# Optimization experiments

Hardware: AMD Instinct MI355X
Metric: run time of the kernel (lower is better)

The kernel has to match this reference:

```python
import jax, jax.numpy as jnp
import numpy as np

N = 50000      # total nodes across batch of graphs
E = 800000     # total directed edges (avg degree 16)
B = 64         # number of graphs
D = 128        # input_dim == hidden_dim
L = 4          # num_layers - 1 GIN layers
OUT = 10
BN_EPS = 1e-5


def setup_inputs() -> dict:
    key = jax.random.key(0)
    ks = jax.random.split(key, 12)
    s = 0.05
    return {
        "x": jax.random.normal(ks[0], (N, D), jnp.float32),
        "pi": jax.random.uniform(ks[1], (B, 25), jnp.float32),
        "eps": jnp.zeros((L,), jnp.float32),
        "mlp_w1": jax.random.normal(ks[2], (L, D, D), jnp.float32) * s,
        "mlp_b1": jnp.zeros((L, D), jnp.float32),
        "mlp_bn_g": jnp.ones((L, D), jnp.float32),
        "mlp_bn_b": jnp.zeros((L, D), jnp.float32),
        "mlp_w2": jax.random.normal(ks[3], (L, D, D), jnp.float32) * s,
        "mlp_b2": jnp.zeros((L, D), jnp.float32),
        "bn_g": jnp.ones((L, D), jnp.float32),
        "bn_b": jnp.zeros((L, D), jnp.float32),
        "attend_w": jax.random.normal(ks[4], (D * (L + 1), 1), jnp.float32) * s,
        "attend_b": jnp.zeros((1,), jnp.float32),
        "pi_w": jax.random.normal(ks[5], (25, 16), jnp.float32) * s,
        "pi_b": jnp.zeros((16,), jnp.float32),
        "out_w": jax.random.normal(ks[6], (D * (L + 1) + 16, OUT), jnp.float32) * s,
        "out_b": jnp.zeros((OUT,), jnp.float32),
        "edge_index": jax.random.randint(ks[7], (2, E), 0, N, dtype=jnp.int32),
        "graph_id": jnp.sort(jax.random.randint(ks[8], (N,), 0, B, dtype=jnp.int32)),
    }


def _bn(z, g, b):
    # BatchNorm1d in training mode over all nodes (axis 0)
    m = z.mean(axis=0)
    v = z.var(axis=0)
    return (z - m) * jax.lax.rsqrt(v + BN_EPS) * g + b


def reference(x, pi, eps, mlp_w1, mlp_b1, mlp_bn_g, mlp_bn_b, mlp_w2, mlp_b2,
              bn_g, bn_b, attend_w, attend_b, pi_w, pi_b, out_w, out_b,
              edge_index, graph_id):
    src, dst = edge_index[0], edge_index[1]
    h = x
    reps = [x]
    for l in range(L):
        # GIN sum aggregation (learn_eps=True: no self-loops in Adj)
        pooled = jax.ops.segment_sum(h[src], dst, num_segments=N)
        pooled = pooled + (1.0 + eps[l]) * h
        # 2-layer MLP: Linear -> BN -> ReLU -> Linear
        z = jax.nn.relu(_bn(pooled @ mlp_w1[l] + mlp_b1[l], mlp_bn_g[l], mlp_bn_b[l]))
        z = z @ mlp_w2[l] + mlp_b2[l]
        # outer BN + ReLU
        h = jax.nn.relu(_bn(z, bn_g[l], bn_b[l]))
        reps.append(h)
    hr = jnp.concatenate(reps, axis=1)               # [N, D*(L+1)]
    # per-graph attention softmax over nodes
    scores = (hr @ attend_w + attend_b)[:, 0]        # [N]
    smax = jax.ops.segment_max(scores, graph_id, num_segments=B)
    e = jnp.exp(scores - smax[graph_id])
    denom = jax.ops.segment_sum(e, graph_id, num_segments=B)
    coef = e / denom[graph_id]
    gemb = jax.ops.segment_sum(hr * coef[:, None], graph_id, num_segments=B)  # [B, D*(L+1)]
    # persistence-image branch (PI computed host-side; treated as input)
    pie = jax.nn.relu(pi @ pi_w + pi_b)              # [B, 16]
    feat = jnp.concatenate([gemb, pie], axis=1)      # [B, D*(L+1)+16]
    return feat @ out_w + out_b                      # [B, OUT]
```

## Files before the change

### kernel.cpp

```cpp
#include <hip/hip_runtime.h>
#include <hip/hip_bf16.h>

#define NN 50000
#define EE 800000
#define BBG 64
#define DD 128
#define LLAY 4
#define HRW 640
#define NOUT 10
#define NXCD 8
#define NBUCK 196
#define BUCKCAP 4608
#define EB 250
#define ECH 3200

typedef __hip_bfloat16 bf16;
typedef __attribute__((ext_vector_type(8))) short short8;
typedef __attribute__((ext_vector_type(4))) float f32x4;

__device__ __forceinline__ float b2f(bf16 v) { return __bfloat162float(v); }
__device__ __forceinline__ float bflo(unsigned u) { return __uint_as_float(u << 16); }
__device__ __forceinline__ float bfhi(unsigned u) { return __uint_as_float(u & 0xffff0000u); }
__device__ __forceinline__ unsigned short f2bs(float v) {
  bf16 h = __float2bfloat16(v);
  unsigned short r; __builtin_memcpy(&r, &h, 2); return r;
}
__device__ __forceinline__ int dtype_of(const void* __restrict__ bng) {
  return (*(const unsigned*)bng == 0x3F800000u) ? 1 : 0;
}
__device__ __forceinline__ float ldf(const void* __restrict__ p, long i, int dt) {
  return dt ? ((const float*)p)[i] : b2f(((const bf16*)p)[i]);
}

__device__ __forceinline__ int xccid() {
  unsigned v;
  asm("s_getreg_b32 %0, hwreg(HW_REG_XCC_ID)" : "=s"(v));
  return (int)(v & (NXCD - 1));
}

__device__ __forceinline__ void fadd_l2(float* p, float v) {
  asm volatile("global_atomic_add_f32 %0, %1, off" :: "v"(p), "v"(v) : "memory");
}

__device__ __forceinline__ int lower_bound_i(const int* __restrict__ a, int n, int key) {
  int lo = 0, hi = n;
  while (lo < hi) { int mid = (lo + hi) >> 1; if (a[mid] < key) lo = mid + 1; else hi = mid; }
  return lo;
}

__global__ __launch_bounds__(256) void gnn_init(const void* __restrict__ x,
                                                bf16* __restrict__ hrb,
                                                const void* __restrict__ w1,
                                                const void* __restrict__ w2,
                                                bf16* __restrict__ w1t,
                                                bf16* __restrict__ w2t,
                                                const void* __restrict__ aw,
                                                float* __restrict__ scores,
                                                const int* __restrict__ ei,
                                                int* __restrict__ bucketCnt,
                                                unsigned* __restrict__ bucketStore,
                                                const void* __restrict__ bng) {
  int dt = dtype_of(bng);
  int tid = threadIdx.x;
  if (blockIdx.x >= 3375) {
    int i = (blockIdx.x - 3375) * 256 + tid;
    int l = i >> 14, rem = i & 16383, n = rem >> 7, k = rem & 127;
    long src = (long)l * 16384 + k * 128 + n;
    w1t[i] = __float2bfloat16(ldf(w1, src, dt));
    w2t[i] = __float2bfloat16(ldf(w2, src, dt));
    return;
  }
  if (blockIdx.x >= 3125) {
    __shared__ int lcnt[NBUCK], gbase[NBUCK];
    int bb = blockIdx.x - 3125;
    int base = bb * ECH;
    if (tid < NBUCK) lcnt[tid] = 0;
    __syncthreads();
    #pragma unroll
    for (int j = 0; j < 13; j++) {
      int k = j * 256 + tid;
      if (k < ECH) {
        int dst = ei[EE + base + k];
        atomicAdd(&lcnt[dst >> 8], 1);
      }
    }
    __syncthreads();
    if (tid < NBUCK) {
      gbase[tid] = atomicAdd(&bucketCnt[tid * 16], lcnt[tid]);
      lcnt[tid] = 0;
    }
    __syncthreads();
    #pragma unroll
    for (int j = 0; j < 13; j++) {
      int k = j * 256 + tid;
      if (k < ECH) {
        int e = base + k;
        int src = ei[e];
        int dst = ei[EE + e];
        int b = dst >> 8;
        int r = atomicAdd(&lcnt[b], 1);
        bucketStore[b * BUCKCAP + gbase[b] + r] =
            (unsigned)src | ((unsigned)(dst & 255) << 16);
      }
    }
    return;
  }
  int n = blockIdx.x * 16 + (tid >> 4);
  int il = tid & 15;
  long base = (long)n * DD + il * 8;
  float v[8];
  if (dt) {
    float4 a0 = *(const float4*)((const float*)x + base);
    float4 a1 = *(const float4*)((const float*)x + base + 4);
    v[0] = a0.x; v[1] = a0.y; v[2] = a0.z; v[3] = a0.w;
    v[4] = a1.x; v[5] = a1.y; v[6] = a1.z; v[7] = a1.w;
  } else {
    uint4 u = *(const uint4*)((const bf16*)x + base);
    v[0] = bflo(u.x); v[1] = bfhi(u.x); v[2] = bflo(u.y); v[3] = bfhi(u.y);
    v[4] = bflo(u.z); v[5] = bfhi(u.z); v[6] = bflo(u.w); v[7] = bfhi(u.w);
  }
  uint4 o;
  o.x = (unsigned)f2bs(v[0]) | ((unsigned)f2bs(v[1]) << 16);
  o.y = (unsigned)f2bs(v[2]) | ((unsigned)f2bs(v[3]) << 16);
  o.z = (unsigned)f2bs(v[4]) | ((unsigned)f2bs(v[5]) << 16);
  o.w = (unsigned)f2bs(v[6]) | ((unsigned)f2bs(v[7]) << 16);
  *(uint4*)(hrb + (size_t)n * HRW + il * 8) = o;
  float ss = 0.f;
  #pragma unroll
  for (int k = 0; k < 8; k++) ss += v[k] * ldf(aw, il * 8 + k, dt);
  ss += __shfl_xor(ss, 1, 64); ss += __shfl_xor(ss, 2, 64);
  ss += __shfl_xor(ss, 4, 64); ss += __shfl_xor(ss, 8, 64);
  if (il == 0) scores[n] = ss;
}

__global__ __launch_bounds__(256) void gnn_csr(const int* __restrict__ bucketCnt,
                                               const unsigned* __restrict__ bucketStore,
                                               int* __restrict__ rowstart,
                                               int* __restrict__ csr_src) {
  __shared__ int cnt[256], dbase[256], buf[256];
  int b = blockIdx.x, tid = threadIdx.x;
  int p = (tid < b) ? bucketCnt[tid * 16] : 0;
  buf[tid] = p;
  __syncthreads();
  for (int s = 128; s > 0; s >>= 1) {
    if (tid < s) buf[tid] += buf[tid + s];
    __syncthreads();
  }
  int start = buf[0];
  int sz = bucketCnt[b * 16];
  __syncthreads();
  cnt[tid] = 0;
  __syncthreads();
  for (int j = 0; j < 18; j++) {
    int k = j * 256 + tid;
    if (k < sz) atomicAdd(&cnt[bucketStore[b * BUCKCAP + k] >> 16], 1);
  }
  __syncthreads();
  int c = cnt[tid];
  buf[tid] = c;
  __syncthreads();
  for (int ofs = 1; ofs < 256; ofs <<= 1) {
    int t = (tid >= ofs) ? buf[tid - ofs] : 0;
    __syncthreads();
    buf[tid] += t;
    __syncthreads();
  }
  dbase[tid] = buf[tid] - c;
  int d = b * 256 + tid;
  if (d <= NN) rowstart[d] = start + buf[tid] - c;
  cnt[tid] = 0;
  __syncthreads();
  for (int j = 0; j < 18; j++) {
    int k = j * 256 + tid;
    if (k < sz) {
      unsigned v = bucketStore[b * BUCKCAP + k];
      int dlo = v >> 16;
      int r = atomicAdd(&cnt[dlo], 1);
      csr_src[start + dbase[dlo] + r] = (int)(v & 0xFFFFu);
    }
  }
}

__device__ __forceinline__ void acc8(float* a, uint4 u) {
  a[0] += bflo(u.x); a[1] += bfhi(u.x);
  a[2] += bflo(u.y); a[3] += bfhi(u.y);
  a[4] += bflo(u.z); a[5] += bfhi(u.z);
  a[6] += bflo(u.w); a[7] += bfhi(u.w);
}

__device__ __forceinline__ float2 statsum(const float* __restrict__ stat, int c) {
  float s = 0.f, q = 0.f;
  #pragma unroll
  for (int k = 0; k < 8; k++) { s += stat[k * 256 + c]; q += stat[k * 256 + 128 + c]; }
  return make_float2(s, q);
}

__global__ __launch_bounds__(512) void gnn_gmg1(const bf16* __restrict__ hrb, int l,
                                                const int* __restrict__ rowstart,
                                                const int* __restrict__ csr_src,
                                                const void* __restrict__ eps,
                                                const bf16* __restrict__ Wt,
                                                const void* __restrict__ bias, int biasOfs,
                                                bf16* __restrict__ out,
                                                float* __restrict__ statOut,
                                                const void* __restrict__ bng) {
  int dt = dtype_of(bng);
  __shared__ __align__(16) unsigned ar[16][68];
  __shared__ int qhead;
  int tid = threadIdx.x, lane = tid & 63;
  int w = tid >> 6;
  int q = lane >> 4, il = lane & 15;
  int r0 = blockIdx.x * 16;
  const bf16* stripe = hrb + l * DD;
  float s = 1.0f + ldf(eps, l, dt);
  if (tid == 0) qhead = 0;
  __syncthreads();

  for (;;) {
    int i;
    if (lane == 0) i = atomicAdd(&qhead, 1);
    i = __shfl(i, 0, 64);
    if (i >= 16) break;
    int n = r0 + i;
    float a[8] = {0.f, 0.f, 0.f, 0.f, 0.f, 0.f, 0.f, 0.f};
    if (q == 0) {
      uint4 u = *(const uint4*)(stripe + (size_t)n * HRW + il * 8);
      a[0] = s * bflo(u.x); a[1] = s * bfhi(u.x);
      a[2] = s * bflo(u.y); a[3] = s * bfhi(u.y);
      a[4] = s * bflo(u.z); a[5] = s * bfhi(u.z);
      a[6] = s * bflo(u.w); a[7] = s * bfhi(u.w);
    }
    int start = rowstart[n], end = rowstart[n + 1];
    for (int base = start; base < end; base += 64) {
      int m = end - base; if (m > 64) m = 64;
      int idx = (base + lane < end) ? csr_src[base + lane] : 0;
      int j = 0;
      for (; j + 16 <= m; j += 16) {
        int s0 = __shfl(idx, j + q, 64);
        int s1 = __shfl(idx, j + 4 + q, 64);
        int s2 = __shfl(idx, j + 8 + q, 64);
        int s3 = __shfl(idx, j + 12 + q, 64);
        uint4 u0 = *(const uint4*)(stripe + (size_t)s0 * HRW + il * 8);
        uint4 u1 = *(const uint4*)(stripe + (size_t)s1 * HRW + il * 8);
        uint4 u2 = *(const uint4*)(stripe + (size_t)s2 * HRW + il * 8);
        uint4 u3 = *(const uint4*)(stripe + (size_t)s3 * HRW + il * 8);
        acc8(a, u0); acc8(a, u1); acc8(a, u2); acc8(a, u3);
      }
      for (; j + 8 <= m; j += 8) {
        int s0 = __shfl(idx, j + q, 64);
        int s1 = __shfl(idx, j + 4 + q, 64);
        uint4 u0 = *(const uint4*)(stripe + (size_t)s0 * HRW + il * 8);
        uint4 u1 = *(const uint4*)(stripe + (size_t)s1 * HRW + il * 8);
        acc8(a, u0); acc8(a, u1);
      }
      for (; j + 4 <= m; j += 4) {
        int src = __shfl(idx, j + q, 64);
        uint4 u = *(const uint4*)(stripe + (size_t)src * HRW + il * 8);
        acc8(a, u);
      }
      for (; j < m; j++) {
        int src = __shfl(idx, j, 64);
        if (q == 0) {
          uint4 u = *(const uint4*)(stripe + (size_t)src * HRW + il * 8);
          acc8(a, u);
        }
      }
    }
    #pragma unroll
    for (int k = 0; k < 8; k++) {
      a[k] += __shfl_xor(a[k], 16, 64);
      a[k] += __shfl_xor(a[k], 32, 64);
    }
    if (q == 0) {
      uint4 o;
      o.x = (unsigned)f2bs(a[0]) | ((unsigned)f2bs(a[1]) << 16);
      o.y = (unsigned)f2bs(a[2]) | ((unsigned)f2bs(a[3]) << 16);
      o.z = (unsigned)f2bs(a[4]) | ((unsigned)f2bs(a[5]) << 16);
      o.w = (unsigned)f2bs(a[6]) | ((unsigned)f2bs(a[7]) << 16);
      *(uint4*)&ar[i][il * 4] = o;
    }
  }
  __syncthreads();

  f32x4 acc = (f32x4){0.f, 0.f, 0.f, 0.f};
  #pragma unroll
  for (int ch = 0; ch < 4; ch++) {
    int k0 = ch * 32 + q * 8;
    uint4 raw = *(const uint4*)&ar[il][ch * 16 + q * 4];
    short8 af;
    __builtin_memcpy(&af, &raw, 16);
    short8 bfv = *(const short8*)(Wt + (w * 16 + il) * DD + k0);
    acc = __builtin_amdgcn_mfma_f32_16x16x32_bf16(af, bfv, acc, 0, 0, 0);
  }
  int col = w * 16 + il;
  float bv = ldf(bias, biasOfs + col, dt);
  float ss = 0.f, qq = 0.f;
  #pragma unroll
  for (int r = 0; r < 4; r++) {
    int row = r0 + q * 4 + r;
    float v = acc[r] + bv;
    out[(size_t)row * DD + col] = __float2bfloat16(v);
    ss += v; qq += v * v;
  }
  ss += __shfl_xor(ss, 16, 64);  ss += __shfl_xor(ss, 32, 64);
  qq += __shfl_xor(qq, 16, 64);  qq += __shfl_xor(qq, 32, 64);
  if (q == 0) {
    int xid = xccid();
    fadd_l2(&statOut[xid * 256 + col], ss);
    fadd_l2(&statOut[xid * 256 + 128 + col], qq);
  }
}

__global__ __launch_bounds__(256) void gnn_mgemm(const bf16* __restrict__ Abf,
                                                 const bf16* __restrict__ Wt,
                                                 const void* __restrict__ bias, int biasOfs,
                                                 bf16* __restrict__ out,
                                                 const float* __restrict__ statIn,
                                                 const void* __restrict__ g,
                                                 const void* __restrict__ bb, int parOfs,
                                                 float* __restrict__ statOut,
                                                 const void* __restrict__ bng) {
  int dt = dtype_of(bng);
  __shared__ float scf[128], shf[128];
  __shared__ float redS[4][128], redQ[4][128];
  int tid = threadIdx.x, w = tid >> 6, lane = tid & 63;
  int q = lane >> 4, il = lane & 15;
  if (tid < 128) {
    const float invN = 1.0f / NN;
    float2 sq = statsum(statIn, tid);
    float m = sq.x * invN;
    float rs = rsqrtf(sq.y * invN - m * m + 1e-5f);
    float gg = ldf(g, parOfs + tid, dt), bv = ldf(bb, parOfs + tid, dt);
    scf[tid] = rs * gg;
    shf[tid] = bv - m * rs * gg;
  }
  __syncthreads();
  int r0 = (blockIdx.x * 4 + w) * 16;
  int arow = r0 + il;
  int arowc = (arow < NN) ? arow : (NN - 1);
  f32x4 acc[8];
  #pragma unroll
  for (int i = 0; i < 8; i++) acc[i] = (f32x4){0.f, 0.f, 0.f, 0.f};
  #pragma unroll
  for (int ch = 0; ch < 4; ch++) {
    int k0 = ch * 32 + q * 8;
    uint4 raw = *(const uint4*)(Abf + (size_t)arowc * DD + k0);
    float4 c0 = *(const float4*)(scf + k0);
    float4 c1 = *(const float4*)(scf + k0 + 4);
    float4 d0 = *(const float4*)(shf + k0);
    float4 d1 = *(const float4*)(shf + k0 + 4);
    short8 af;
    af[0] = (short)f2bs(fmaxf(bflo(raw.x) * c0.x + d0.x, 0.f));
    af[1] = (short)f2bs(fmaxf(bfhi(raw.x) * c0.y + d0.y, 0.f));
    af[2] = (short)f2bs(fmaxf(bflo(raw.y) * c0.z + d0.z, 0.f));
    af[3] = (short)f2bs(fmaxf(bfhi(raw.y) * c0.w + d0.w, 0.f));
    af[4] = (short)f2bs(fmaxf(bflo(raw.z) * c1.x + d1.x, 0.f));
    af[5] = (short)f2bs(fmaxf(bfhi(raw.z) * c1.y + d1.y, 0.f));
    af[6] = (short)f2bs(fmaxf(bflo(raw.w) * c1.z + d1.z, 0.f));
    af[7] = (short)f2bs(fmaxf(bfhi(raw.w) * c1.w + d1.w, 0.f));
    #pragma unroll
    for (int ct = 0; ct < 8; ct++) {
      short8 bfv = *(const short8*)(Wt + (ct * 16 + il) * DD + k0);
      acc[ct] = __builtin_amdgcn_mfma_f32_16x16x32_bf16(af, bfv, acc[ct], 0, 0, 0);
    }
  }
  #pragma unroll
  for (int ct = 0; ct < 8; ct++) {
    int col = ct * 16 + il;
    float bv = ldf(bias, biasOfs + col, dt);
    float s = 0.f, qq = 0.f;
    #pragma unroll
    for (int r = 0; r < 4; r++) {
      int row = r0 + q * 4 + r;
      float v = acc[ct][r] + bv;
      if (row < NN) {
        out[(size_t)row * DD + col] = __float2bfloat16(v);
        s += v; qq += v * v;
      }
    }
    s += __shfl_xor(s, 16, 64);  s += __shfl_xor(s, 32, 64);
    qq += __shfl_xor(qq, 16, 64); qq += __shfl_xor(qq, 32, 64);
    if (q == 0) { redS[w][col] = s; redQ[w][col] = qq; }
  }
  __syncthreads();
  int xid = xccid();
  if (tid < 128) {
    float v = redS[0][tid] + redS[1][tid] + redS[2][tid] + redS[3][tid];
    fadd_l2(&statOut[xid * 256 + tid], v);
  } else {
    int c = tid - 128;
    float v = redQ[0][c] + redQ[1][c] + redQ[2][c] + redQ[3][c];
    fadd_l2(&statOut[xid * 256 + 128 + c], v);
  }
}

__global__ __launch_bounds__(256) void gnn_bn_relu(const bf16* __restrict__ z2,
                                                   const float* __restrict__ stat,
                                                   const void* __restrict__ g,
                                                   const void* __restrict__ bb, int parOfs,
                                                   bf16* __restrict__ hrb, int stripe,
                                                   const void* __restrict__ aw,
                                                   float* __restrict__ scores,
                                                   const void* __restrict__ bng) {
  int dt = dtype_of(bng);
  __shared__ float scf[128], shf[128], awf[128];
  int tid = threadIdx.x;
  if (tid < 128) {
    const float invN = 1.0f / NN;
    float2 sq = statsum(stat, tid);
    float m = sq.x * invN;
    float rs = rsqrtf(sq.y * invN - m * m + 1e-5f);
    float gg = ldf(g, parOfs + tid, dt), bv = ldf(bb, parOfs + tid, dt);
    scf[tid] = rs * gg;
    shf[tid] = bv - m * rs * gg;
    awf[tid] = ldf(aw, stripe * DD + tid, dt);
  }
  __syncthreads();
  int n = blockIdx.x * 16 + (tid >> 4);
  int il = tid & 15;
  int c0 = il * 8;
  uint4 u = *(const uint4*)(z2 + (size_t)n * DD + c0);
  float v[8];
  v[0] = bflo(u.x); v[1] = bfhi(u.x); v[2] = bflo(u.y); v[3] = bfhi(u.y);
  v[4] = bflo(u.z); v[5] = bfhi(u.z); v[6] = bflo(u.w); v[7] = bfhi(u.w);
  float ss = 0.f;
  #pragma unroll
  for (int k = 0; k < 8; k++) {
    v[k] = fmaxf(v[k] * scf[c0 + k] + shf[c0 + k], 0.f);
    ss += v[k] * awf[c0 + k];
  }
  uint4 o;
  o.x = (unsigned)f2bs(v[0]) | ((unsigned)f2bs(v[1]) << 16);
  o.y = (unsigned)f2bs(v[2]) | ((unsigned)f2bs(v[3]) << 16);
  o.z = (unsigned)f2bs(v[4]) | ((unsigned)f2bs(v[5]) << 16);
  o.w = (unsigned)f2bs(v[6]) | ((unsigned)f2bs(v[7]) << 16);
  *(uint4*)(hrb + (size_t)n * HRW + stripe * DD + c0) = o;
  ss += __shfl_xor(ss, 1, 64); ss += __shfl_xor(ss, 2, 64);
  ss += __shfl_xor(ss, 4, 64); ss += __shfl_xor(ss, 8, 64);
  if (il == 0) scores[n] += ss;
}

__global__ __launch_bounds__(128) void gnn_gemb(const bf16* __restrict__ hrb,
                                                const float* __restrict__ scores,
                                                const int* __restrict__ gid,
                                                float* __restrict__ gembp) {
  int b = blockIdx.x / 40;
  int part = blockIdx.x % 40;
  int chunk = part % 5;
  int slice = part / 5;
  int tid = threadIdx.x;
  int start = lower_bound_i(gid, NN, b);
  int end = lower_bound_i(gid, NN, b + 1);
  __shared__ float red[128];
  float mx = -3.4e38f;
  for (int n = start + tid; n < end; n += 128) mx = fmaxf(mx, scores[n]);
  red[tid] = mx;
  __syncthreads();
  for (int s = 64; s > 0; s >>= 1) {
    if (tid < s) red[tid] = fmaxf(red[tid], red[tid + s]);
    __syncthreads();
  }
  float smax = red[0];
  __syncthreads();
  float sum = 0.f;
  for (int n = start + tid; n < end; n += 128) sum += __expf(scores[n] - smax);
  red[tid] = sum;
  __syncthreads();
  for (int s = 64; s > 0; s >>= 1) {
    if (tid < s) red[tid] += red[tid + s];
    __syncthreads();
  }
  float denom = red[0];
  float inv = (denom > 0.f) ? 1.0f / denom : 0.f;
  int c = chunk * 128 + tid;
  float acc = 0.f;
  for (int n = start + slice; n < end; n += 8)
    acc += b2f(hrb[(size_t)n * HRW + c]) * __expf(scores[n] - smax) * inv;
  gembp[((size_t)slice * BBG + b) * HRW + c] = acc;
}

__global__ __launch_bounds__(64) void gnn_final(const float* __restrict__ gembp,
                                                const void* __restrict__ pi,
                                                const void* __restrict__ piw,
                                                const void* __restrict__ pib,
                                                const void* __restrict__ ow,
                                                const void* __restrict__ ob,
                                                void* __restrict__ out,
                                                const void* __restrict__ bng) {
  int dt = dtype_of(bng);
  int b = blockIdx.x;
  int t = threadIdx.x;
  __shared__ float pie[16];
  if (t < 16) {
    float s = ldf(pib, t, dt);
    for (int i = 0; i < 25; i++) s += ldf(pi, b * 25 + i, dt) * ldf(piw, i * 16 + t, dt);
    pie[t] = fmaxf(s, 0.f);
  }
  __syncthreads();
  float fv[11];
  #pragma unroll
  for (int i = 0; i < 11; i++) {
    int c = t + i * 64;
    float f = 0.f;
    if (c < HRW) {
      #pragma unroll
      for (int s = 0; s < 8; s++) f += gembp[((size_t)s * BBG + b) * HRW + c];
    } else if (c < HRW + 16) {
      f = pie[c - HRW];
    }
    fv[i] = f;
  }
  for (int o = 0; o < NOUT; o++) {
    float s = 0.f;
    #pragma unroll
    for (int i = 0; i < 11; i++) {
      int c = t + i * 64;
      if (c < HRW + 16) s += fv[i] * ldf(ow, (long)c * NOUT + o, dt);
    }
    #pragma unroll
    for (int m = 32; m > 0; m >>= 1) s += __shfl_xor(s, m, 64);
    if (t == 0) {
      float r = s + ldf(ob, o, dt);
      if (dt) ((float*)out)[b * NOUT + o] = r;
      else ((bf16*)out)[b * NOUT + o] = __float2bfloat16(r);
    }
  }
}

extern "C" void kernel_launch(void* const* d_in, const int* in_sizes, int n_in,
                              void* d_out, int out_size, void* d_ws, size_t ws_size,
                              hipStream_t stream) {
  const void* x    = d_in[0];
  const void* pi   = d_in[1];
  const void* eps  = d_in[2];
  const void* w1   = d_in[3];
  const void* b1   = d_in[4];
  const void* bng  = d_in[5];
  const void* bnb  = d_in[6];
  const void* w2   = d_in[7];
  const void* b2   = d_in[8];
  const void* obng = d_in[9];
  const void* obnb = d_in[10];
  const void* aw   = d_in[11];
  const void* piw  = d_in[13];
  const void* pib  = d_in[14];
  const void* ow   = d_in[15];
  const void* ob   = d_in[16];
  const int*  ei   = (const int*)d_in[17];
  const int*  gid  = (const int*)d_in[18];

  bf16*  hrb      = (bf16*)d_ws;
  bf16*  z1       = hrb + (size_t)NN * HRW;
  bf16*  z2       = z1 + (size_t)NN * DD;
  bf16*  w1t      = z2 + (size_t)NN * DD;
  bf16*  w2t      = w1t + LLAY * DD * DD;
  float* statbufs = (float*)(w2t + LLAY * DD * DD);
  int*   bucketCnt= (int*)(statbufs + 8 * 2048);
  size_t zeroBytes = (size_t)(8 * 2048 + NBUCK * 16) * 4;
  float* gembp    = (float*)(bucketCnt + NBUCK * 16);
  float* scores   = gembp + (size_t)8 * BBG * HRW;
  int*   rowstart = (int*)(scores + NN);
  unsigned* bucketStore = (unsigned*)(rowstart + NN + 1);
  int*   csr_src  = (int*)(bucketStore + (size_t)NBUCK * BUCKCAP);

  hipMemsetAsync(statbufs, 0, zeroBytes, stream);
  gnn_init<<<3631, 256, 0, stream>>>(x, hrb, w1, w2, w1t, w2t, aw, scores,
                                     ei, bucketCnt, bucketStore, bng);
  gnn_csr<<<NBUCK, 256, 0, stream>>>(bucketCnt, bucketStore, rowstart, csr_src);

  for (int l = 0; l < LLAY; l++) {
    float* statA = statbufs + (l * 2 + 0) * 2048;
    float* statB = statbufs + (l * 2 + 1) * 2048;
    gnn_gmg1<<<NN / 16, 512, 0, stream>>>(hrb, l, rowstart, csr_src, eps,
                                          w1t + l * DD * DD, b1, l * DD,
                                          z1, statA, bng);
    gnn_mgemm<<<782, 256, 0, stream>>>(z1, w2t + l * DD * DD, b2, l * DD,
                                       z2, statA, bng, bnb, l * DD,
                                       statB, bng);
    gnn_bn_relu<<<NN / 16, 256, 0, stream>>>(z2, statB, obng, obnb, l * DD,
                                             hrb, l + 1, aw, scores, bng);
  }

  gnn_gemb<<<BBG * 40, 128, 0, stream>>>(hrb, scores, gid, gembp);
  gnn_final<<<BBG, 64, 0, stream>>>(gembp, pi, piw, pib, ow, ob, d_out, bng);
}
```

Baseline: 536.8 us.

## Software-pipeline GIN neighbor gather and vectorize attention pooling

The aggregation kernel now caches rowstart in shared memory and prefetches the next node's index and CSR chunk while the current node is processed. The 16-neighbor gather is double-buffered so loads for the next group are issued before the current one is accumulated. The pooling kernel switches to 8-wide bf16 vector loads with 16 node slices and a quarter as many blocks, and the final kernel reduces 16 partials instead of 8. The CSR entries also pack the low destination bits into the upper half of each index, which every reader must now mask off. The costs are more registers, which may lower occupancy, and a larger partial buffer.

```diff
diff --git a/kernel.cpp b/kernel.cpp
--- a/kernel.cpp
+++ b/kernel.cpp
@@ -176,9 +176,16 @@
       unsigned v = bucketStore[b * BUCKCAP + k];
       int dlo = v >> 16;
       int r = atomicAdd(&cnt[dlo], 1);
-      csr_src[start + dbase[dlo] + r] = (int)(v & 0xFFFFu);
-    }
-  }
+      csr_src[start + dbase[dlo] + r] = (int)(v & 0xFFFFu) | ((dlo & 15) << 16);
+    }
+  }
+}
+
+__device__ __forceinline__ float2 statsum(const float* __restrict__ stat, int c) {
+  float s = 0.f, q = 0.f;
+  #pragma unroll
+  for (int k = 0; k < 8; k++) { s += stat[k * 256 + c]; q += stat[k * 256 + 128 + c]; }
+  return make_float2(s, q);
 }
 
 __device__ __forceinline__ void acc8(float* a, uint4 u) {
@@ -188,11 +195,17 @@
   a[6] += bflo(u.w); a[7] += bfhi(u.w);
 }
 
-__device__ __forceinline__ float2 statsum(const float* __restrict__ stat, int c) {
-  float s = 0.f, q = 0.f;
-  #pragma unroll
-  for (int k = 0; k < 8; k++) { s += stat[k * 256 + c]; q += stat[k * 256 + 128 + c]; }
-  return make_float2(s, q);
+__device__ __forceinline__ void ldg16(const bf16* __restrict__ stripe, int idx, int j,
+                                      int q, int il,
+                                      uint4& u0, uint4& u1, uint4& u2, uint4& u3) {
+  int s0 = __shfl(idx, j + q, 64) & 0xFFFF;
+  int s1 = __shfl(idx, j + 4 + q, 64) & 0xFFFF;
+  int s2 = __shfl(idx, j + 8 + q, 64) & 0xFFFF;
+  int s3 = __shfl(idx, j + 12 + q, 64) & 0xFFFF;
+  u0 = *(const uint4*)(stripe + (size_t)s0 * HRW + il * 8);
+  u1 = *(const uint4*)(stripe + (size_t)s1 * HRW + il * 8);
+  u2 = *(const uint4*)(stripe + (size_t)s2 * HRW + il * 8);
+  u3 = *(const uint4*)(stripe + (size_t)s3 * HRW + il * 8);
 }
 
 __global__ __launch_bounds__(512) void gnn_gmg1(const bf16* __restrict__ hrb, int l,
@@ -206,6 +219,7 @@
                                                 const void* __restrict__ bng) {
   int dt = dtype_of(bng);
   __shared__ __align__(16) unsigned ar[16][68];
+  __shared__ int rs[17];
   __shared__ int qhead;
   int tid = threadIdx.x, lane = tid & 63;
   int w = tid >> 6;
@@ -213,58 +227,79 @@
   int r0 = blockIdx.x * 16;
   const bf16* stripe = hrb + l * DD;
   float s = 1.0f + ldf(eps, l, dt);
+  if (tid < 17) rs[tid] = rowstart[r0 + tid];
   if (tid == 0) qhead = 0;
   __syncthreads();
 
-  for (;;) {
-    int i;
-    if (lane == 0) i = atomicAdd(&qhead, 1);
-    i = __shfl(i, 0, 64);
-    if (i >= 16) break;
-    int n = r0 + i;
+  int i, start = 0, end = 0, idx = 0;
+  {
+    int v;
+    if (lane == 0) v = atomicAdd(&qhead, 1);
+    i = __shfl(v, 0, 64);
+    if (i < 16) {
+      start = rs[i]; end = rs[i + 1];
+      idx = (start + lane < end) ? csr_src[start + lane] : 0;
+    }
+  }
+  while (i < 16) {
+    int i_nxt;
+    {
+      int v;
+      if (lane == 0) v = atomicAdd(&qhead, 1);
+      i_nxt = __shfl(v, 0, 64);
+    }
+    int start_n = 0, end_n = 0, idx_n = 0;
+    if (i_nxt < 16) {
+      start_n = rs[i_nxt]; end_n = rs[i_nxt + 1];
+      idx_n = (start_n + lane < end_n) ? csr_src[start_n + lane] : 0;
+    }
+
     float a[8] = {0.f, 0.f, 0.f, 0.f, 0.f, 0.f, 0.f, 0.f};
     if (q == 0) {
-      uint4 u = *(const uint4*)(stripe + (size_t)n * HRW + il * 8);
+      uint4 u = *(const uint4*)(stripe + (size_t)(r0 + i) * HRW + il * 8);
       a[0] = s * bflo(u.x); a[1] = s * bfhi(u.x);
       a[2] = s * bflo(u.y); a[3] = s * bfhi(u.y);
       a[4] = s * bflo(u.z); a[5] = s * bfhi(u.z);
       a[6] = s * bflo(u.w); a[7] = s * bfhi(u.w);
     }
-    int start = rowstart[n], end = rowstart[n + 1];
-    for (int base = start; base < end; base += 64) {
-      int m = end - base; if (m > 64) m = 64;
-      int idx = (base + lane < end) ? csr_src[base + lane] : 0;
+    int p = start;
+    int m = end - p; if (m > 64) m = 64;
+    for (;;) {
       int j = 0;
-      for (; j + 16 <= m; j += 16) {
-        int s0 = __shfl(idx, j + q, 64);
-        int s1 = __shfl(idx, j + 4 + q, 64);
-        int s2 = __shfl(idx, j + 8 + q, 64);
-        int s3 = __shfl(idx, j + 12 + q, 64);
-        uint4 u0 = *(const uint4*)(stripe + (size_t)s0 * HRW + il * 8);
-        uint4 u1 = *(const uint4*)(stripe + (size_t)s1 * HRW + il * 8);
-        uint4 u2 = *(const uint4*)(stripe + (size_t)s2 * HRW + il * 8);
-        uint4 u3 = *(const uint4*)(stripe + (size_t)s3 * HRW + il * 8);
-        acc8(a, u0); acc8(a, u1); acc8(a, u2); acc8(a, u3);
+      if (m >= 16) {
+        uint4 c0, c1, c2, c3;
+        ldg16(stripe, idx, 0, q, il, c0, c1, c2, c3);
+        for (j = 16; j + 16 <= m; j += 16) {
+          uint4 n0, n1, n2, n3;
+          ldg16(stripe, idx, j, q, il, n0, n1, n2, n3);
+          acc8(a, c0); acc8(a, c1); acc8(a, c2); acc8(a, c3);
+          c0 = n0; c1 = n1; c2 = n2; c3 = n3;
+        }
+        acc8(a, c0); acc8(a, c1); acc8(a, c2); acc8(a, c3);
       }
       for (; j + 8 <= m; j += 8) {
-        int s0 = __shfl(idx, j + q, 64);
-        int s1 = __shfl(idx, j + 4 + q, 64);
+        int s0 = __shfl(idx, j + q, 64) & 0xFFFF;
+        int s1 = __shfl(idx, j + 4 + q, 64) & 0xFFFF;
         uint4 u0 = *(const uint4*)(stripe + (size_t)s0 * HRW + il * 8);
         uint4 u1 = *(const uint4*)(stripe + (size_t)s1 * HRW + il * 8);
         acc8(a, u0); acc8(a, u1);
       }
       for (; j + 4 <= m; j += 4) {
-        int src = __shfl(idx, j + q, 64);
-        uint4 u = *(const uint4*)(stripe + (size_t)src * HRW + il * 8);
-        acc8(a, u);
+        int s0 = __shfl(idx, j + q, 64) & 0xFFFF;
+        uint4 u0 = *(const uint4*)(stripe + (size_t)s0 * HRW + il * 8);
+        acc8(a, u0);
       }
       for (; j < m; j++) {
-        int src = __shfl(idx, j, 64);
+        int s0 = __shfl(idx, j, 64) & 0xFFFF;
         if (q == 0) {
-          uint4 u = *(const uint4*)(stripe + (size_t)src * HRW + il * 8);
-          acc8(a, u);
+          uint4 u0 = *(const uint4*)(stripe + (size_t)s0 * HRW + il * 8);
+          acc8(a, u0);
         }
       }
+      p += m;
+      if (p >= end) break;
+      m = end - p; if (m > 64) m = 64;
+      idx = (p + lane < end) ? csr_src[p + lane] : 0;
     }
     #pragma unroll
     for (int k = 0; k < 8; k++) {
@@ -279,6 +314,7 @@
       o.w = (unsigned)f2bs(a[6]) | ((unsigned)f2bs(a[7]) << 16);
       *(uint4*)&ar[i][il * 4] = o;
     }
+    i = i_nxt; start = start_n; end = end_n; idx = idx_n;
   }
   __syncthreads();
 
@@ -286,9 +322,9 @@
   #pragma unroll
   for (int ch = 0; ch < 4; ch++) {
     int k0 = ch * 32 + q * 8;
-    uint4 raw = *(const uint4*)&ar[il][ch * 16 + q * 4];
+    uint4 raw2 = *(const uint4*)&ar[il][ch * 16 + q * 4];
     short8 af;
-    __builtin_memcpy(&af, &raw, 16);
+    __builtin_memcpy(&af, &raw2, 16);
     short8 bfv = *(const short8*)(Wt + (w * 16 + il) * DD + k0);
     acc = __builtin_amdgcn_mfma_f32_16x16x32_bf16(af, bfv, acc, 0, 0, 0);
   }
@@ -444,10 +480,10 @@
                                                 const float* __restrict__ scores,
                                                 const int* __restrict__ gid,
                                                 float* __restrict__ gembp) {
-  int b = blockIdx.x / 40;
-  int part = blockIdx.x % 40;
-  int chunk = part % 5;
-  int slice = part / 5;
+  int b = blockIdx.x / 10;
+  int part = blockIdx.x % 10;
+  int chunk = part >> 1;
+  int half = part & 1;
   int tid = threadIdx.x;
   int start = lower_bound_i(gid, NN, b);
   int end = lower_bound_i(gid, NN, b + 1);
@@ -472,11 +508,25 @@
   }
   float denom = red[0];
   float inv = (denom > 0.f) ? 1.0f / denom : 0.f;
-  int c = chunk * 128 + tid;
-  float acc = 0.f;
-  for (int n = start + slice; n < end; n += 8)
-    acc += b2f(hrb[(size_t)n * HRW + c]) * __expf(scores[n] - smax) * inv;
-  gembp[((size_t)slice * BBG + b) * HRW + c] = acc;
+  int cg = tid & 15;
+  int sl = half * 8 + (tid >> 4);
+  int c0 = chunk * 128 + cg * 8;
+  float acc[8] = {0.f, 0.f, 0.f, 0.f, 0.f, 0.f, 0.f, 0.f};
+  for (int n = start + sl; n < end; n += 16) {
+    float wgt = __expf(scores[n] - smax) * inv;
+    uint4 u = *(const uint4*)(hrb + (size_t)n * HRW + c0);
+    acc[0] = fmaf(bflo(u.x), wgt, acc[0]);
+    acc[1] = fmaf(bfhi(u.x), wgt, acc[1]);
+    acc[2] = fmaf(bflo(u.y), wgt, acc[2]);
+    acc[3] = fmaf(bfhi(u.y), wgt, acc[3]);
+    acc[4] = fmaf(bflo(u.z), wgt, acc[4]);
+    acc[5] = fmaf(bfhi(u.z), wgt, acc[5]);
+    acc[6] = fmaf(bflo(u.w), wgt, acc[6]);
+    acc[7] = fmaf(bfhi(u.w), wgt, acc[7]);
+  }
+  float* dst = gembp + ((size_t)sl * BBG + b) * HRW + c0;
+  *(float4*)dst = make_float4(acc[0], acc[1], acc[2], acc[3]);
+  *(float4*)(dst + 4) = make_float4(acc[4], acc[5], acc[6], acc[7]);
 }
 
 __global__ __launch_bounds__(64) void gnn_final(const float* __restrict__ gembp,
@@ -504,7 +554,7 @@
     float f = 0.f;
     if (c < HRW) {
       #pragma unroll
-      for (int s = 0; s < 8; s++) f += gembp[((size_t)s * BBG + b) * HRW + c];
+      for (int s = 0; s < 16; s++) f += gembp[((size_t)s * BBG + b) * HRW + c];
     } else if (c < HRW + 16) {
       f = pie[c - HRW];
     }
@@ -558,7 +608,7 @@
   int*   bucketCnt= (int*)(statbufs + 8 * 2048);
   size_t zeroBytes = (size_t)(8 * 2048 + NBUCK * 16) * 4;
   float* gembp    = (float*)(bucketCnt + NBUCK * 16);
-  float* scores   = gembp + (size_t)8 * BBG * HRW;
+  float* scores   = gembp + (size_t)16 * BBG * HRW;
   int*   rowstart = (int*)(scores + NN);
   unsigned* bucketStore = (unsigned*)(rowstart + NN + 1);
   int*   csr_src  = (int*)(bucketStore + (size_t)NBUCK * BUCKCAP);
@@ -581,6 +631,6 @@
                                              hrb, l + 1, aw, scores, bng);
   }
 
-  gnn_gemb<<<BBG * 40, 128, 0, stream>>>(hrb, scores, gid, gembp);
+  gnn_gemb<<<BBG * 10, 128, 0, stream>>>(hrb, scores, gid, gembp);
   gnn_final<<<BBG, 64, 0, stream>>>(gembp, pi, piw, pib, ow, ob, d_out, bng);
 }
```

Result: no change. 530.4 us (-1.2%).
